# Optimization experiments

Hardware: AMD Instinct MI355X
Metric: run time of the kernel (lower is better)

The kernel has to match this reference:

```python
import jax, jax.numpy as jnp
import numpy as np

EPS = 1e-06


def _create_circular_masks(h, w):
    # Faithful to the torch code: y spans width, x spans height -> mask shape (w, h).
    # Only used with square feature maps (h == w), matching the module's implicit assumption.
    cen_w, cen_h = w // 2, h // 2
    y = np.arange(-cen_w, w - cen_w).reshape(-1, 1)
    x = np.arange(-cen_h, h - cen_h).reshape(1, -1)
    y2, x2 = y * y, x * x
    r2 = x2 + y2
    masks = [r2 <= 0]
    max_r = int(np.sqrt(r2.max())) + 1
    quadrants = [(1, 1), (-1, 1), (1, -1), (-1, -1)]  # (sign_x, sign_y)
    for radius in range(1, max_r):
        lo, hi = (radius - 1) ** 2, radius ** 2
        for sx, sy in quadrants:
            quad = (sx * x >= 0) & (sy * y >= 0)
            masks.append((r2 > lo) & (r2 <= hi) & quad)  # ring mask
            masks.append((r2 <= hi) & quad)              # circle mask
    return np.stack(masks).astype(np.float32)  # [M, w, h] == [M, h, w] for square maps


def _l2_normalize(v):
    # v: [B, C]; torch norms over dim=1 with eps added to the norm
    return v / (jnp.linalg.norm(v, axis=1, keepdims=True) + EPS)


def setup_inputs() -> dict:
    key = jax.random.key(0)
    x = jax.random.normal(key, (32, 1024, 28, 28), dtype=jnp.float32)
    return {"x": x}


def reference(x) -> jnp.ndarray:
    B, C, H, W = x.shape
    masks = jnp.asarray(_create_circular_masks(H, W))  # [M, H, W] static constant
    # Global descriptor: max-pool over full map, then channel-wise L2 normalize.
    v = _l2_normalize(jnp.max(x, axis=(2, 3)))  # [B, C]
    # Accumulate masked-max descriptors; scan over the (fixed) mask set keeps
    # peak memory at one masked feature map instead of M of them.
    def step(acc, mask):
        vt = jnp.max(x * mask, axis=(2, 3))  # masked max-pool (zeros included, as in torch)
        return acc + _l2_normalize(vt), None
    v, _ = jax.lax.scan(step, v, masks)
    return v[:, :, None, None]  # [B, C, 1, 1] to match F.max_pool2d output shape
```

## Files before the change

### kernel.cpp

```cpp
#include <hip/hip_runtime.h>
#include <math.h>

#define B_DIM 32
#define C_DIM 1024
#define MAP 784
#define NMASK 153
#define NTERM 154
#define NROW 192
#define NBIN 77
#define DUMMY_BIN 77
#define MAX1 28
#define MAX2 6
#define MPW 8

struct Sched {
    unsigned short off1[MAX1][64];
    unsigned short off2[MAX2][64];
    unsigned char  binA[64];
    unsigned char  binB[64];
    bool ok;
};

constexpr Sched build_sched() {
    Sched S{};
    S.ok = true;
    short px[NBIN][40] = {};
    int   n[NBIN] = {};
    for (int i = 0; i < 28; ++i)
        for (int j = 0; j < 28; ++j) {
            int dy = i - 14, dx = j - 14, r2 = dx * dx + dy * dy;
            int p = i * 28 + j;
            if (r2 == 0) { px[0][n[0]++] = (short)p; continue; }
            if (r2 > 361) continue;
            int r = 0; while (r * r < r2) ++r;
            const int sx[4] = {1, -1, 1, -1}, sy[4] = {1, 1, -1, -1};
            for (int q = 0; q < 4; ++q)
                if (sx[q] * dx >= 0 && sy[q] * dy >= 0) {
                    int b = 1 + q * 19 + (r - 1);
                    if (n[b] >= 40) { S.ok = false; continue; }
                    px[b][n[b]++] = (short)p;
                }
        }
    int ord[NBIN] = {};
    for (int k = 0; k < NBIN; ++k) ord[k] = k;
    for (int a = 0; a < NBIN; ++a) {
        int best = a;
        for (int c = a + 1; c < NBIN; ++c)
            if (n[ord[c]] > n[ord[best]]) best = c;
        int t = ord[a]; ord[a] = ord[best]; ord[best] = t;
    }
    for (int l = 0; l < 64; ++l) {
        S.binA[l] = (unsigned char)ord[l];
        S.binB[l] = (l >= 51) ? (unsigned char)ord[64 + (l - 51)]
                              : (unsigned char)DUMMY_BIN;
        if (n[ord[l]] > MAX1) S.ok = false;
        if (l >= 51 && n[ord[64 + (l - 51)]] > MAX2) S.ok = false;
    }
    {
        bool used[64][40] = {};
        for (int s = 0; s < MAX1; ++s) {
            int bankcnt[32] = {};
            for (int l = 0; l < 64; ++l) {
                int bin = S.binA[l], cnt = n[bin];
                int bestp = 0, bestload = 1 << 30; bool haveUnused = false;
                for (int t = 0; t < cnt; ++t)
                    if (!used[l][t]) {
                        int load = bankcnt[px[bin][t] % 32];
                        if (!haveUnused || load < bestload) { haveUnused = true; bestload = load; bestp = t; }
                    }
                if (!haveUnused)
                    for (int t = 0; t < cnt; ++t) {
                        int load = bankcnt[px[bin][t] % 32];
                        if (load < bestload) { bestload = load; bestp = t; }
                    }
                int p = px[bin][bestp];
                if (haveUnused) used[l][bestp] = true;
                S.off1[s][l] = (unsigned short)(p * 4);
                bankcnt[p % 32]++;
            }
        }
        for (int l = 0; l < 64; ++l)
            for (int t = 0; t < n[S.binA[l]]; ++t)
                if (!used[l][t]) S.ok = false;
    }
    {
        bool used[64][40] = {};
        for (int s = 0; s < MAX2; ++s) {
            int bankcnt[32] = {};
            for (int l = 0; l < 64; ++l) {
                if (S.binB[l] == DUMMY_BIN) {
                    S.off2[s][l] = (unsigned short)((l % 32) * 4);
                    continue;
                }
                int bin = S.binB[l], cnt = n[bin];
                int bestp = 0, bestload = 1 << 30; bool haveUnused = false;
                for (int t = 0; t < cnt; ++t)
                    if (!used[l][t]) {
                        int load = bankcnt[px[bin][t] % 32];
                        if (!haveUnused || load < bestload) { haveUnused = true; bestload = load; bestp = t; }
                    }
                if (!haveUnused)
                    for (int t = 0; t < cnt; ++t) {
                        int load = bankcnt[px[bin][t] % 32];
                        if (load < bestload) { bestload = load; bestp = t; }
                    }
                int p = px[bin][bestp];
                if (haveUnused) used[l][bestp] = true;
                S.off2[s][l] = (unsigned short)(p * 4);
                bankcnt[p % 32]++;
            }
        }
        for (int l = 0; l < 64; ++l)
            if (S.binB[l] != DUMMY_BIN)
                for (int t = 0; t < n[S.binB[l]]; ++t)
                    if (!used[l][t]) S.ok = false;
    }
    return S;
}

static_assert(build_sched().ok, "schedule overflow / unplaced pixel");
__constant__ Sched d_sched = build_sched();

__device__ __forceinline__ int term_addr(int k) {
    if (k == 0) return 0;
    if (k >= NMASK) return DUMMY_BIN;
    int t = k - 1, q = (t >> 1) & 3, rm1 = t >> 3;
    return (t & 1) ? 78 + q * 19 + rm1
                   : 1 + q * 19 + rm1;
}

__global__ __launch_bounds__(256) void cac_k1(const float* __restrict__ x,
                                              float* __restrict__ vt,
                                              float* __restrict__ partial) {
    __shared__ __align__(16) float smap[4][MAP];
    __shared__ float sbuf[4][160];
    __shared__ float ssqred[4][NROW];

    const int wave = threadIdx.x >> 6;
    const int lane = threadIdx.x & 63;
    const int pair0 = blockIdx.x * 32 + wave * MPW;

    const int linA = lane % 19;
    const bool inA = lane < 57, inB = lane < 19;
    const int rbA = 1 + lane;
    const int rbB = inB ? 58 + lane : DUMMY_BIN;
    const int a0 = term_addr(lane);
    const int a1 = term_addr(lane + 64);
    const int a2 = term_addr(lane + 128);

    const float4 NEG4 = make_float4(-INFINITY, -INFINITY, -INFINITY, -INFINITY);
    const float4* xp4 = (const float4*)(x + (size_t)pair0 * MAP);
    float4 t0 = xp4[lane], t1 = xp4[64 + lane], t2 = xp4[128 + lane];
    float4 t3 = NEG4;
    if (lane < 4) t3 = xp4[192 + lane];

    float* smw = smap[wave];
    float* sbw = sbuf[wave];
    float sq0 = 0.0f, sq1 = 0.0f, sq2 = 0.0f;

    #pragma unroll
    for (int m = 0; m < MPW; ++m) {
        ((float4*)smw)[lane]       = t0;
        ((float4*)smw)[64 + lane]  = t1;
        ((float4*)smw)[128 + lane] = t2;
        if (lane < 4) ((float4*)smw)[192 + lane] = t3;
        float gmax = fmaxf(fmaxf(fmaxf(t0.x, t0.y), fmaxf(t0.z, t0.w)),
                           fmaxf(fmaxf(t1.x, t1.y), fmaxf(t1.z, t1.w)));
        gmax = fmaxf(gmax, fmaxf(fmaxf(t2.x, t2.y), fmaxf(t2.z, t2.w)));
        gmax = fmaxf(gmax, fmaxf(fmaxf(t3.x, t3.y), fmaxf(t3.z, t3.w)));

        if (m < MPW - 1) {
            const float4* np4 = (const float4*)(x + (size_t)(pair0 + m + 1) * MAP);
            t0 = np4[lane]; t1 = np4[64 + lane]; t2 = np4[128 + lane];
            t3 = NEG4;
            if (lane < 4) t3 = np4[192 + lane];
        }
        __builtin_amdgcn_wave_barrier();

        const char* base = (const char*)smw;
        float m1 = 0.0f, m2v = 0.0f;
        #pragma unroll
        for (int s = 0; s < MAX1; ++s)
            m1 = fmaxf(m1, *(const float*)(base + d_sched.off1[s][lane]));
        #pragma unroll
        for (int s = 0; s < MAX2; ++s)
            m2v = fmaxf(m2v, *(const float*)(base + d_sched.off2[s][lane]));
        sbw[d_sched.binA[lane]] = m1;
        sbw[d_sched.binB[lane]] = m2v;

        #pragma unroll
        for (int off = 32; off; off >>= 1)
            gmax = fmaxf(gmax, __shfl_xor(gmax, off, 64));
        __builtin_amdgcn_wave_barrier();

        float cval = sbw[0];
        float rA = fmaxf(sbw[rbA], cval);
        float rB = fmaxf(sbw[rbB], cval);
        #pragma unroll
        for (int s = 1; s <= 16; s <<= 1) {
            float uA = __shfl_up(rA, s, 64);
            float uB = __shfl_up(rB, s, 64);
            if (linA >= s) rA = fmaxf(rA, uA);
            if (lane >= s) rB = fmaxf(rB, uB);
        }
        if (inA) sbw[78 + lane] = rA;
        if (inB) sbw[135 + lane] = rB;
        __builtin_amdgcn_wave_barrier();

        float r0 = sbw[a0];
        float r1 = sbw[a1];
        float r2 = sbw[a2];
        r2 = (lane == 25) ? gmax : (lane < 26 ? r2 : 0.0f);

        float* rowp = vt + (size_t)(pair0 + m) * NROW;
        rowp[lane]       = r0;
        rowp[64 + lane]  = r1;
        rowp[128 + lane] = r2;
        sq0 += r0 * r0; sq1 += r1 * r1; sq2 += r2 * r2;
        __builtin_amdgcn_wave_barrier();
    }

    ssqred[wave][lane]       = sq0;
    ssqred[wave][lane + 64]  = sq1;
    ssqred[wave][lane + 128] = sq2;
    __syncthreads();
    if (threadIdx.x < NROW) {
        int t = threadIdx.x;
        partial[(size_t)blockIdx.x * NROW + t] =
            ssqred[0][t] + ssqred[1][t] + ssqred[2][t] + ssqred[3][t];
    }
}

__global__ __launch_bounds__(256) void cac_k2(const float* __restrict__ vt,
                                              const float* __restrict__ partial,
                                              float* __restrict__ out) {
    __shared__ __align__(16) float sinv[NROW];
    const int b = blockIdx.x >> 3;

    if (threadIdx.x < NROW) {
        int t = threadIdx.x;
        const float* p = partial + (size_t)(b * 32) * NROW + t;
        float s = 0.0f;
        #pragma unroll
        for (int j = 0; j < 32; ++j) s += p[j * NROW];
        sinv[t] = (t < NTERM) ? 1.0f / (sqrtf(s) + 1e-6f) : 0.0f;
    }
    __syncthreads();

    const int local = threadIdx.x >> 1;
    const int half  = threadIdx.x & 1;
    const int pair  = blockIdx.x * 128 + local;
    const float4* row = (const float4*)(vt + (size_t)pair * NROW + half * 96);
    const float4* w4  = (const float4*)sinv + half * 24;
    float acc = 0.0f;
    #pragma unroll
    for (int i = 0; i < 24; ++i) {
        float4 v = row[i], w = w4[i];
        acc += v.x * w.x + v.y * w.y + v.z * w.z + v.w * w.w;
    }
    acc += __shfl_xor(acc, 1, 64);
    if (!half) out[pair] = acc;
}

extern "C" void kernel_launch(void* const* d_in, const int* in_sizes, int n_in,
                              void* d_out, int out_size, void* d_ws, size_t ws_size,
                              hipStream_t stream) {
    const float* x = (const float*)d_in[0];
    float* out = (float*)d_out;

    float* vt      = (float*)d_ws;
    float* partial = vt + (size_t)B_DIM * C_DIM * NROW;

    cac_k1<<<1024, 256, 0, stream>>>(x, vt, partial);
    cac_k2<<<256, 256, 0, stream>>>(vt, partial, out);
}
```

Before: 162.2 us.

## Fuse both kernels with a grid-wide atomic barrier, keep per-pair terms in registers

```diff
diff --git a/kernel.cpp b/kernel.cpp
--- a/kernel.cpp
+++ b/kernel.cpp
@@ -12,6 +12,7 @@
 #define MAX1 28
 #define MAX2 6
 #define MPW 8
+#define NBLK 1024
 
 struct Sched {
     unsigned short off1[MAX1][64];
@@ -129,16 +130,20 @@
                    : 1 + q * 19 + rm1;
 }
 
-__global__ __launch_bounds__(256) void cac_k1(const float* __restrict__ x,
-                                              float* __restrict__ vt,
-                                              float* __restrict__ partial) {
+__global__ __launch_bounds__(256, 4) void cac_fused(const float* __restrict__ x,
+                                                    float* __restrict__ partial,
+                                                    unsigned* __restrict__ barrier_cnt,
+                                                    float* __restrict__ out) {
     __shared__ __align__(16) float smap[4][MAP];
     __shared__ float sbuf[4][160];
     __shared__ float ssqred[4][NROW];
+    __shared__ __align__(16) float sinv[NROW];
 
     const int wave = threadIdx.x >> 6;
     const int lane = threadIdx.x & 63;
-    const int pair0 = blockIdx.x * 32 + wave * MPW;
+    const int bk = blockIdx.x;
+    const int pair0 = bk * 32 + wave * MPW;
+    const int b = bk >> 5;
 
     const int linA = lane % 19;
     const bool inA = lane < 57, inB = lane < 19;
@@ -157,6 +162,7 @@
     float* smw = smap[wave];
     float* sbw = sbuf[wave];
     float sq0 = 0.0f, sq1 = 0.0f, sq2 = 0.0f;
+    float r0a[MPW], r1a[MPW], r2a[MPW];
 
     #pragma unroll
     for (int m = 0; m < MPW; ++m) {
@@ -211,11 +217,7 @@
         float r1 = sbw[a1];
         float r2 = sbw[a2];
         r2 = (lane == 25) ? gmax : (lane < 26 ? r2 : 0.0f);
-
-        float* rowp = vt + (size_t)(pair0 + m) * NROW;
-        rowp[lane]       = r0;
-        rowp[64 + lane]  = r1;
-        rowp[128 + lane] = r2;
+        r0a[m] = r0; r1a[m] = r1; r2a[m] = r2;
         sq0 += r0 * r0; sq1 += r1 * r1; sq2 += r2 * r2;
         __builtin_amdgcn_wave_barrier();
     }
@@ -226,16 +228,21 @@
     __syncthreads();
     if (threadIdx.x < NROW) {
         int t = threadIdx.x;
-        partial[(size_t)blockIdx.x * NROW + t] =
+        partial[(size_t)bk * NROW + t] =
             ssqred[0][t] + ssqred[1][t] + ssqred[2][t] + ssqred[3][t];
     }
-}
-
-__global__ __launch_bounds__(256) void cac_k2(const float* __restrict__ vt,
-                                              const float* __restrict__ partial,
-                                              float* __restrict__ out) {
-    __shared__ __align__(16) float sinv[NROW];
-    const int b = blockIdx.x >> 3;
+
+    __threadfence();
+    __syncthreads();
+    if (threadIdx.x == 0) {
+        __hip_atomic_fetch_add(barrier_cnt, 1u, __ATOMIC_RELEASE,
+                               __HIP_MEMORY_SCOPE_AGENT);
+        while (__hip_atomic_load(barrier_cnt, __ATOMIC_ACQUIRE,
+                                 __HIP_MEMORY_SCOPE_AGENT) < (unsigned)NBLK)
+            __builtin_amdgcn_s_sleep(2);
+    }
+    __syncthreads();
+    __threadfence();
 
     if (threadIdx.x < NROW) {
         int t = threadIdx.x;
@@ -247,19 +254,16 @@
     }
     __syncthreads();
 
-    const int local = threadIdx.x >> 1;
-    const int half  = threadIdx.x & 1;
-    const int pair  = blockIdx.x * 128 + local;
-    const float4* row = (const float4*)(vt + (size_t)pair * NROW + half * 96);
-    const float4* w4  = (const float4*)sinv + half * 24;
-    float acc = 0.0f;
+    float w0 = sinv[lane];
+    float w1 = sinv[64 + lane];
+    float w2 = sinv[128 + lane];
     #pragma unroll
-    for (int i = 0; i < 24; ++i) {
-        float4 v = row[i], w = w4[i];
-        acc += v.x * w.x + v.y * w.y + v.z * w.z + v.w * w.w;
-    }
-    acc += __shfl_xor(acc, 1, 64);
-    if (!half) out[pair] = acc;
+    for (int m = 0; m < MPW; ++m) {
+        float d = r0a[m] * w0 + r1a[m] * w1 + r2a[m] * w2;
+        #pragma unroll
+        for (int off = 32; off; off >>= 1) d += __shfl_xor(d, off, 64);
+        if (lane == 0) out[pair0 + m] = d;
+    }
 }
 
 extern "C" void kernel_launch(void* const* d_in, const int* in_sizes, int n_in,
@@ -268,9 +272,9 @@
     const float* x = (const float*)d_in[0];
     float* out = (float*)d_out;
 
-    float* vt      = (float*)d_ws;
-    float* partial = vt + (size_t)B_DIM * C_DIM * NROW;
-
-    cac_k1<<<1024, 256, 0, stream>>>(x, vt, partial);
-    cac_k2<<<256, 256, 0, stream>>>(vt, partial, out);
-}
+    unsigned* barrier_cnt = (unsigned*)d_ws;
+    float* partial = (float*)((char*)d_ws + 256);
+
+    hipMemsetAsync(d_ws, 0, 256, stream);
+    cac_fused<<<NBLK, 256, 0, stream>>>(x, partial, barrier_cnt, out);
+}
```

After: 485.2 us. +199.1%, slower.

## Gather bin pixels as float2 pairs and reduce norms with atomics

Applied to the files above, without the earlier changes.

```diff
diff --git a/kernel.cpp b/kernel.cpp
--- a/kernel.cpp
+++ b/kernel.cpp
@@ -9,15 +9,16 @@
 #define NROW 192
 #define NBIN 77
 #define DUMMY_BIN 77
-#define MAX1 28
-#define MAX2 6
+#define NW1 28
+#define NW2 8
 #define MPW 8
 
 struct Sched {
-    unsigned short off1[MAX1][64];
-    unsigned short off2[MAX2][64];
+    unsigned short w1[NW1][64];
+    unsigned short w2[NW2][64];
     unsigned char  binA[64];
     unsigned char  binB[64];
+    int ns1, ns2;
     bool ok;
 };
 
@@ -53,73 +54,106 @@
         S.binA[l] = (unsigned char)ord[l];
         S.binB[l] = (l >= 51) ? (unsigned char)ord[64 + (l - 51)]
                               : (unsigned char)DUMMY_BIN;
-        if (n[ord[l]] > MAX1) S.ok = false;
-        if (l >= 51 && n[ord[64 + (l - 51)]] > MAX2) S.ok = false;
-    }
+        if (n[ord[l]] < 1) S.ok = false;
+    }
+
+    int wlist[64][NW1] = {};
+    int wcnt[64] = {};
+    for (int l = 0; l < 64; ++l) {
+        bool has[784] = {};
+        int bin = S.binA[l];
+        for (int t = 0; t < n[bin]; ++t) has[px[bin][t]] = true;
+        int c = 0;
+        for (int w = 0; w < 392; ++w) {
+            bool ex = has[2 * w], ey = has[2 * w + 1];
+            if (ex || ey) {
+                if (c >= NW1) { S.ok = false; break; }
+                wlist[l][c++] = w | (ex ? 0x4000 : 0) | (ey ? 0x8000 : 0);
+            }
+        }
+        wcnt[l] = c;
+        if (c < 1) S.ok = false;
+    }
+    int ns1 = 0;
+    for (int l = 0; l < 64; ++l) if (wcnt[l] > ns1) ns1 = wcnt[l];
+    S.ns1 = ns1;
     {
-        bool used[64][40] = {};
-        for (int s = 0; s < MAX1; ++s) {
-            int bankcnt[32] = {};
+        bool used[64][NW1] = {};
+        for (int s = 0; s < ns1; ++s) {
+            int pcnt[16] = {};
             for (int l = 0; l < 64; ++l) {
-                int bin = S.binA[l], cnt = n[bin];
-                int bestp = 0, bestload = 1 << 30; bool haveUnused = false;
+                int cnt = wcnt[l], bestt = -1, bestload = 1 << 30;
                 for (int t = 0; t < cnt; ++t)
                     if (!used[l][t]) {
-                        int load = bankcnt[px[bin][t] % 32];
-                        if (!haveUnused || load < bestload) { haveUnused = true; bestload = load; bestp = t; }
+                        int load = pcnt[(wlist[l][t] & 0x1FF) % 16];
+                        if (load < bestload) { bestload = load; bestt = t; }
                     }
-                if (!haveUnused)
-                    for (int t = 0; t < cnt; ++t) {
-                        int load = bankcnt[px[bin][t] % 32];
-                        if (load < bestload) { bestload = load; bestp = t; }
-                    }
-                int p = px[bin][bestp];
-                if (haveUnused) used[l][bestp] = true;
-                S.off1[s][l] = (unsigned short)(p * 4);
-                bankcnt[p % 32]++;
+                int enc;
+                if (bestt >= 0) { used[l][bestt] = true; enc = wlist[l][bestt]; }
+                else enc = wlist[l][s % cnt];
+                S.w1[s][l] = (unsigned short)enc;
+                pcnt[(enc & 0x1FF) % 16]++;
             }
         }
         for (int l = 0; l < 64; ++l)
-            for (int t = 0; t < n[S.binA[l]]; ++t)
+            for (int t = 0; t < wcnt[l]; ++t)
                 if (!used[l][t]) S.ok = false;
     }
+
+    int wlist2[64][NW2] = {};
+    int wcnt2[64] = {};
+    for (int l = 51; l < 64; ++l) {
+        bool has[784] = {};
+        int bin = S.binB[l];
+        for (int t = 0; t < n[bin]; ++t) has[px[bin][t]] = true;
+        int c = 0;
+        for (int w = 0; w < 392; ++w) {
+            bool ex = has[2 * w], ey = has[2 * w + 1];
+            if (ex || ey) {
+                if (c >= NW2) { S.ok = false; break; }
+                wlist2[l][c++] = w | (ex ? 0x4000 : 0) | (ey ? 0x8000 : 0);
+            }
+        }
+        wcnt2[l] = c;
+        if (c < 1) S.ok = false;
+    }
+    int ns2 = 1;
+    for (int l = 51; l < 64; ++l) if (wcnt2[l] > ns2) ns2 = wcnt2[l];
+    S.ns2 = ns2;
     {
-        bool used[64][40] = {};
-        for (int s = 0; s < MAX2; ++s) {
-            int bankcnt[32] = {};
+        bool used[64][NW2] = {};
+        for (int s = 0; s < ns2; ++s) {
+            int pcnt[16] = {};
             for (int l = 0; l < 64; ++l) {
-                if (S.binB[l] == DUMMY_BIN) {
-                    S.off2[s][l] = (unsigned short)((l % 32) * 4);
+                if (l < 51) {
+                    S.w2[s][l] = (unsigned short)((l * 13 + s * 5) % 392);
                     continue;
                 }
-                int bin = S.binB[l], cnt = n[bin];
-                int bestp = 0, bestload = 1 << 30; bool haveUnused = false;
+                int cnt = wcnt2[l], bestt = -1, bestload = 1 << 30;
                 for (int t = 0; t < cnt; ++t)
                     if (!used[l][t]) {
-                        int load = bankcnt[px[bin][t] % 32];
-                        if (!haveUnused || load < bestload) { haveUnused = true; bestload = load; bestp = t; }
+                        int load = pcnt[(wlist2[l][t] & 0x1FF) % 16];
+                        if (load < bestload) { bestload = load; bestt = t; }
                     }
-                if (!haveUnused)
-                    for (int t = 0; t < cnt; ++t) {
-                        int load = bankcnt[px[bin][t] % 32];
-                        if (load < bestload) { bestload = load; bestp = t; }
-                    }
-                int p = px[bin][bestp];
-                if (haveUnused) used[l][bestp] = true;
-                S.off2[s][l] = (unsigned short)(p * 4);
-                bankcnt[p % 32]++;
+                int enc;
+                if (bestt >= 0) { used[l][bestt] = true; enc = wlist2[l][bestt]; }
+                else enc = wlist2[l][s % cnt];
+                S.w2[s][l] = (unsigned short)enc;
+                pcnt[(enc & 0x1FF) % 16]++;
             }
         }
-        for (int l = 0; l < 64; ++l)
-            if (S.binB[l] != DUMMY_BIN)
-                for (int t = 0; t < n[S.binB[l]]; ++t)
-                    if (!used[l][t]) S.ok = false;
+        for (int l = 51; l < 64; ++l)
+            for (int t = 0; t < wcnt2[l]; ++t)
+                if (!used[l][t]) S.ok = false;
     }
     return S;
 }
 
-static_assert(build_sched().ok, "schedule overflow / unplaced pixel");
-__constant__ Sched d_sched = build_sched();
+static constexpr Sched h_sched = build_sched();
+static_assert(h_sched.ok, "schedule overflow / empty bin / unplaced window");
+constexpr int NS1 = h_sched.ns1;
+constexpr int NS2 = h_sched.ns2;
+__constant__ Sched d_sched = h_sched;
 
 __device__ __forceinline__ int term_addr(int k) {
     if (k == 0) return 0;
@@ -131,7 +165,7 @@
 
 __global__ __launch_bounds__(256) void cac_k1(const float* __restrict__ x,
                                               float* __restrict__ vt,
-                                              float* __restrict__ partial) {
+                                              float* __restrict__ normsq) {
     __shared__ __align__(16) float smap[4][MAP];
     __shared__ float sbuf[4][160];
     __shared__ float ssqred[4][NROW];
@@ -180,11 +214,19 @@
         const char* base = (const char*)smw;
         float m1 = 0.0f, m2v = 0.0f;
         #pragma unroll
-        for (int s = 0; s < MAX1; ++s)
-            m1 = fmaxf(m1, *(const float*)(base + d_sched.off1[s][lane]));
+        for (int s = 0; s < NS1; ++s) {
+            unsigned e = d_sched.w1[s][lane];
+            float2 v = *(const float2*)(base + (e & 0x1FFu) * 8);
+            m1 = fmaxf(m1, fmaxf((e & 0x4000u) ? v.x : 0.0f,
+                                 (e & 0x8000u) ? v.y : 0.0f));
+        }
         #pragma unroll
-        for (int s = 0; s < MAX2; ++s)
-            m2v = fmaxf(m2v, *(const float*)(base + d_sched.off2[s][lane]));
+        for (int s = 0; s < NS2; ++s) {
+            unsigned e = d_sched.w2[s][lane];
+            float2 v = *(const float2*)(base + (e & 0x1FFu) * 8);
+            m2v = fmaxf(m2v, fmaxf((e & 0x4000u) ? v.x : 0.0f,
+                                   (e & 0x8000u) ? v.y : 0.0f));
+        }
         sbw[d_sched.binA[lane]] = m1;
         sbw[d_sched.binB[lane]] = m2v;
 
@@ -226,24 +268,21 @@
     __syncthreads();
     if (threadIdx.x < NROW) {
         int t = threadIdx.x;
-        partial[(size_t)blockIdx.x * NROW + t] =
-            ssqred[0][t] + ssqred[1][t] + ssqred[2][t] + ssqred[3][t];
+        float s = ssqred[0][t] + ssqred[1][t] + ssqred[2][t] + ssqred[3][t];
+        atomicAdd(&normsq[(blockIdx.x >> 5) * NROW + t], s);
     }
 }
 
 __global__ __launch_bounds__(256) void cac_k2(const float* __restrict__ vt,
-                                              const float* __restrict__ partial,
+                                              const float* __restrict__ normsq,
                                               float* __restrict__ out) {
     __shared__ __align__(16) float sinv[NROW];
     const int b = blockIdx.x >> 3;
 
     if (threadIdx.x < NROW) {
-        int t = threadIdx.x;
-        const float* p = partial + (size_t)(b * 32) * NROW + t;
-        float s = 0.0f;
-        #pragma unroll
-        for (int j = 0; j < 32; ++j) s += p[j * NROW];
-        sinv[t] = (t < NTERM) ? 1.0f / (sqrtf(s) + 1e-6f) : 0.0f;
+        float s = normsq[b * NROW + threadIdx.x];
+        sinv[threadIdx.x] = (threadIdx.x < NTERM) ? 1.0f / (sqrtf(s) + 1e-6f)
+                                                  : 0.0f;
     }
     __syncthreads();
 
@@ -268,9 +307,10 @@
     const float* x = (const float*)d_in[0];
     float* out = (float*)d_out;
 
-    float* vt      = (float*)d_ws;
-    float* partial = vt + (size_t)B_DIM * C_DIM * NROW;
-
-    cac_k1<<<1024, 256, 0, stream>>>(x, vt, partial);
-    cac_k2<<<256, 256, 0, stream>>>(vt, partial, out);
-}
+    float* normsq = (float*)d_ws;
+    float* vt     = normsq + (size_t)B_DIM * NROW;
+
+    hipMemsetAsync(normsq, 0, (size_t)B_DIM * NROW * sizeof(float), stream);
+    cac_k1<<<1024, 256, 0, stream>>>(x, vt, normsq);
+    cac_k2<<<256, 256, 0, stream>>>(vt, normsq, out);
+}
```

Measured after the change: 171.0 us. 5.4% more time.

## Process two maps per wave iteration and shrink intermediate row to 160

Applied to the files above, without the earlier changes.

```diff
diff --git a/kernel.cpp b/kernel.cpp
--- a/kernel.cpp
+++ b/kernel.cpp
@@ -6,7 +6,7 @@
 #define MAP 784
 #define NMASK 153
 #define NTERM 154
-#define NROW 192
+#define NROW 160
 #define NBIN 77
 #define DUMMY_BIN 77
 #define MAX1 28
@@ -129,11 +129,11 @@
                    : 1 + q * 19 + rm1;
 }
 
-__global__ __launch_bounds__(256) void cac_k1(const float* __restrict__ x,
-                                              float* __restrict__ vt,
-                                              float* __restrict__ partial) {
-    __shared__ __align__(16) float smap[4][MAP];
-    __shared__ float sbuf[4][160];
+__global__ __launch_bounds__(256, 4) void cac_k1(const float* __restrict__ x,
+                                                 float* __restrict__ vt,
+                                                 float* __restrict__ partial) {
+    __shared__ __align__(16) float smap[4][2 * MAP];
+    __shared__ float sbuf[4][2][160];
     __shared__ float ssqred[4][NROW];
 
     const int wave = threadIdx.x >> 6;
@@ -149,80 +149,107 @@
     const int a2 = term_addr(lane + 128);
 
     const float4 NEG4 = make_float4(-INFINITY, -INFINITY, -INFINITY, -INFINITY);
-    const float4* xp4 = (const float4*)(x + (size_t)pair0 * MAP);
-    float4 t0 = xp4[lane], t1 = xp4[64 + lane], t2 = xp4[128 + lane];
-    float4 t3 = NEG4;
-    if (lane < 4) t3 = xp4[192 + lane];
-
-    float* smw = smap[wave];
-    float* sbw = sbuf[wave];
+    const float4* pA = (const float4*)(x + (size_t)pair0 * MAP);
+    const float4* pB = (const float4*)(x + (size_t)(pair0 + 1) * MAP);
+    float4 A0 = pA[lane], A1 = pA[64 + lane], A2 = pA[128 + lane], A3 = NEG4;
+    float4 B0 = pB[lane], B1 = pB[64 + lane], B2 = pB[128 + lane], B3 = NEG4;
+    if (lane < 4) { A3 = pA[192 + lane]; B3 = pB[192 + lane]; }
+
+    float* smA = smap[wave];
+    float* smB = smap[wave] + MAP;
+    float* sbA = sbuf[wave][0];
+    float* sbB = sbuf[wave][1];
     float sq0 = 0.0f, sq1 = 0.0f, sq2 = 0.0f;
 
     #pragma unroll
-    for (int m = 0; m < MPW; ++m) {
-        ((float4*)smw)[lane]       = t0;
-        ((float4*)smw)[64 + lane]  = t1;
-        ((float4*)smw)[128 + lane] = t2;
-        if (lane < 4) ((float4*)smw)[192 + lane] = t3;
-        float gmax = fmaxf(fmaxf(fmaxf(t0.x, t0.y), fmaxf(t0.z, t0.w)),
-                           fmaxf(fmaxf(t1.x, t1.y), fmaxf(t1.z, t1.w)));
-        gmax = fmaxf(gmax, fmaxf(fmaxf(t2.x, t2.y), fmaxf(t2.z, t2.w)));
-        gmax = fmaxf(gmax, fmaxf(fmaxf(t3.x, t3.y), fmaxf(t3.z, t3.w)));
-
-        if (m < MPW - 1) {
-            const float4* np4 = (const float4*)(x + (size_t)(pair0 + m + 1) * MAP);
-            t0 = np4[lane]; t1 = np4[64 + lane]; t2 = np4[128 + lane];
-            t3 = NEG4;
-            if (lane < 4) t3 = np4[192 + lane];
+    for (int c = 0; c < MPW / 2; ++c) {
+        ((float4*)smA)[lane] = A0; ((float4*)smA)[64 + lane] = A1;
+        ((float4*)smA)[128 + lane] = A2;
+        ((float4*)smB)[lane] = B0; ((float4*)smB)[64 + lane] = B1;
+        ((float4*)smB)[128 + lane] = B2;
+        if (lane < 4) { ((float4*)smA)[192 + lane] = A3;
+                        ((float4*)smB)[192 + lane] = B3; }
+        float gmaxA = fmaxf(fmaxf(fmaxf(A0.x, A0.y), fmaxf(A0.z, A0.w)),
+                            fmaxf(fmaxf(A1.x, A1.y), fmaxf(A1.z, A1.w)));
+        gmaxA = fmaxf(gmaxA, fmaxf(fmaxf(A2.x, A2.y), fmaxf(A2.z, A2.w)));
+        gmaxA = fmaxf(gmaxA, fmaxf(fmaxf(A3.x, A3.y), fmaxf(A3.z, A3.w)));
+        float gmaxB = fmaxf(fmaxf(fmaxf(B0.x, B0.y), fmaxf(B0.z, B0.w)),
+                            fmaxf(fmaxf(B1.x, B1.y), fmaxf(B1.z, B1.w)));
+        gmaxB = fmaxf(gmaxB, fmaxf(fmaxf(B2.x, B2.y), fmaxf(B2.z, B2.w)));
+        gmaxB = fmaxf(gmaxB, fmaxf(fmaxf(B3.x, B3.y), fmaxf(B3.z, B3.w)));
+
+        if (c < MPW / 2 - 1) {
+            const float4* nA = (const float4*)(x + (size_t)(pair0 + 2 * c + 2) * MAP);
+            const float4* nB = (const float4*)(x + (size_t)(pair0 + 2 * c + 3) * MAP);
+            A0 = nA[lane]; A1 = nA[64 + lane]; A2 = nA[128 + lane]; A3 = NEG4;
+            B0 = nB[lane]; B1 = nB[64 + lane]; B2 = nB[128 + lane]; B3 = NEG4;
+            if (lane < 4) { A3 = nA[192 + lane]; B3 = nB[192 + lane]; }
         }
         __builtin_amdgcn_wave_barrier();
 
-        const char* base = (const char*)smw;
-        float m1 = 0.0f, m2v = 0.0f;
-        #pragma unroll
-        for (int s = 0; s < MAX1; ++s)
-            m1 = fmaxf(m1, *(const float*)(base + d_sched.off1[s][lane]));
-        #pragma unroll
-        for (int s = 0; s < MAX2; ++s)
-            m2v = fmaxf(m2v, *(const float*)(base + d_sched.off2[s][lane]));
-        sbw[d_sched.binA[lane]] = m1;
-        sbw[d_sched.binB[lane]] = m2v;
-
-        #pragma unroll
-        for (int off = 32; off; off >>= 1)
-            gmax = fmaxf(gmax, __shfl_xor(gmax, off, 64));
+        const char* baseA = (const char*)smA;
+        const char* baseB = (const char*)smB;
+        float m1A = 0.0f, m2A = 0.0f, m1B = 0.0f, m2B = 0.0f;
+        #pragma unroll
+        for (int s = 0; s < MAX1; ++s) {
+            unsigned off = d_sched.off1[s][lane];
+            m1A = fmaxf(m1A, *(const float*)(baseA + off));
+            m1B = fmaxf(m1B, *(const float*)(baseB + off));
+        }
+        #pragma unroll
+        for (int s = 0; s < MAX2; ++s) {
+            unsigned off = d_sched.off2[s][lane];
+            m2A = fmaxf(m2A, *(const float*)(baseA + off));
+            m2B = fmaxf(m2B, *(const float*)(baseB + off));
+        }
+        sbA[d_sched.binA[lane]] = m1A;
+        sbA[d_sched.binB[lane]] = m2A;
+        sbB[d_sched.binA[lane]] = m1B;
+        sbB[d_sched.binB[lane]] = m2B;
+
+        #pragma unroll
+        for (int off = 32; off; off >>= 1) {
+            gmaxA = fmaxf(gmaxA, __shfl_xor(gmaxA, off, 64));
+            gmaxB = fmaxf(gmaxB, __shfl_xor(gmaxB, off, 64));
+        }
         __builtin_amdgcn_wave_barrier();
 
-        float cval = sbw[0];
-        float rA = fmaxf(sbw[rbA], cval);
-        float rB = fmaxf(sbw[rbB], cval);
+        float cvA = sbA[0], cvB = sbB[0];
+        float rA1 = fmaxf(sbA[rbA], cvA);
+        float rA2 = fmaxf(sbA[rbB], cvA);
+        float rB1 = fmaxf(sbB[rbA], cvB);
+        float rB2 = fmaxf(sbB[rbB], cvB);
         #pragma unroll
         for (int s = 1; s <= 16; s <<= 1) {
-            float uA = __shfl_up(rA, s, 64);
-            float uB = __shfl_up(rB, s, 64);
-            if (linA >= s) rA = fmaxf(rA, uA);
-            if (lane >= s) rB = fmaxf(rB, uB);
-        }
-        if (inA) sbw[78 + lane] = rA;
-        if (inB) sbw[135 + lane] = rB;
+            float uA1 = __shfl_up(rA1, s, 64), uA2 = __shfl_up(rA2, s, 64);
+            float uB1 = __shfl_up(rB1, s, 64), uB2 = __shfl_up(rB2, s, 64);
+            if (linA >= s) { rA1 = fmaxf(rA1, uA1); rB1 = fmaxf(rB1, uB1); }
+            if (lane >= s) { rA2 = fmaxf(rA2, uA2); rB2 = fmaxf(rB2, uB2); }
+        }
+        if (inA) { sbA[78 + lane] = rA1; sbB[78 + lane] = rB1; }
+        if (inB) { sbA[135 + lane] = rA2; sbB[135 + lane] = rB2; }
         __builtin_amdgcn_wave_barrier();
 
-        float r0 = sbw[a0];
-        float r1 = sbw[a1];
-        float r2 = sbw[a2];
-        r2 = (lane == 25) ? gmax : (lane < 26 ? r2 : 0.0f);
-
-        float* rowp = vt + (size_t)(pair0 + m) * NROW;
-        rowp[lane]       = r0;
-        rowp[64 + lane]  = r1;
-        rowp[128 + lane] = r2;
-        sq0 += r0 * r0; sq1 += r1 * r1; sq2 += r2 * r2;
+        float r0A = sbA[a0], r1A = sbA[a1], r2A = sbA[a2];
+        float r0B = sbB[a0], r1B = sbB[a1], r2B = sbB[a2];
+        r2A = (lane == 25) ? gmaxA : (lane < 26 ? r2A : 0.0f);
+        r2B = (lane == 25) ? gmaxB : (lane < 26 ? r2B : 0.0f);
+
+        float* rowA = vt + (size_t)(pair0 + 2 * c) * NROW;
+        float* rowB = rowA + NROW;
+        rowA[lane] = r0A;      rowB[lane] = r0B;
+        rowA[64 + lane] = r1A; rowB[64 + lane] = r1B;
+        if (lane < 32) { rowA[128 + lane] = r2A; rowB[128 + lane] = r2B; }
+
+        sq0 += r0A * r0A + r0B * r0B;
+        sq1 += r1A * r1A + r1B * r1B;
+        sq2 += r2A * r2A + r2B * r2B;
         __builtin_amdgcn_wave_barrier();
     }
 
-    ssqred[wave][lane]       = sq0;
-    ssqred[wave][lane + 64]  = sq1;
-    ssqred[wave][lane + 128] = sq2;
+    ssqred[wave][lane]      = sq0;
+    ssqred[wave][64 + lane] = sq1;
+    if (lane < 32) ssqred[wave][128 + lane] = sq2;
     __syncthreads();
     if (threadIdx.x < NROW) {
         int t = threadIdx.x;
@@ -250,11 +277,11 @@
     const int local = threadIdx.x >> 1;
     const int half  = threadIdx.x & 1;
     const int pair  = blockIdx.x * 128 + local;
-    const float4* row = (const float4*)(vt + (size_t)pair * NROW + half * 96);
-    const float4* w4  = (const float4*)sinv + half * 24;
+    const float4* row = (const float4*)(vt + (size_t)pair * NROW + half * 80);
+    const float4* w4  = (const float4*)(sinv + half * 80);
     float acc = 0.0f;
     #pragma unroll
-    for (int i = 0; i < 24; ++i) {
+    for (int i = 0; i < 20; ++i) {
         float4 v = row[i], w = w4[i];
         acc += v.x * w.x + v.y * w.y + v.z * w.z + v.w * w.w;
     }
```

Result: slower. 176.1 us (+8.5%).
